# Performance work log

Measured on AMD Instinct MI355X. Metric: run time of the kernel, lower is better.

## Reference

```python
import jax, jax.numpy as jnp
import numpy as np

DIM = 384
HEADS = 12
POS_DIM = (DIM // 4) // 4  # DynamicPosBias: pos_dim = (dim//4)//4 = 24
B_WIN = 64
GH = GW = GD = 8
N_TOK = GH * GW * GD  # 512
NG = 8  # num windows sharing one mask


def _ln(x, g, b):
    m = jnp.mean(x, axis=-1, keepdims=True)
    v = jnp.var(x, axis=-1, keepdims=True)
    return (x - m) / jnp.sqrt(v + 1e-5) * g + b


def setup_inputs() -> dict:
    key = jax.random.key(0)
    ks = jax.random.split(key, 8)
    s = 0.02
    inp = {
        "x": jax.random.normal(ks[0], (B_WIN, N_TOK, DIM), jnp.float32),
        "H": GH, "W": GW, "D": GD,
        "mask": jnp.zeros((NG, N_TOK, N_TOK), jnp.float32),
        "qkv_w": jax.random.normal(ks[1], (DIM, 3 * DIM), jnp.float32) * s,
        "qkv_b": jnp.zeros((3 * DIM,), jnp.float32),
        "proj_w": jax.random.normal(ks[2], (DIM, DIM), jnp.float32) * s,
        "proj_b": jnp.zeros((DIM,), jnp.float32),
        "pos_proj_w": jax.random.normal(ks[3], (3, POS_DIM), jnp.float32) * s,
        "pos_proj_b": jnp.zeros((POS_DIM,), jnp.float32),
        "ln1_g": jnp.ones((POS_DIM,), jnp.float32), "ln1_b": jnp.zeros((POS_DIM,), jnp.float32),
        "pos1_w": jax.random.normal(ks[4], (POS_DIM, POS_DIM), jnp.float32) * s,
        "pos1_b": jnp.zeros((POS_DIM,), jnp.float32),
        "ln2_g": jnp.ones((POS_DIM,), jnp.float32), "ln2_b": jnp.zeros((POS_DIM,), jnp.float32),
        "pos2_w": jax.random.normal(ks[5], (POS_DIM, POS_DIM), jnp.float32) * s,
        "pos2_b": jnp.zeros((POS_DIM,), jnp.float32),
        "ln3_g": jnp.ones((POS_DIM,), jnp.float32), "ln3_b": jnp.zeros((POS_DIM,), jnp.float32),
        "pos3_w": jax.random.normal(ks[6], (POS_DIM, HEADS), jnp.float32) * s,
        "pos3_b": jnp.zeros((HEADS,), jnp.float32),
    }
    return inp


def reference(x, H, W, D, mask, qkv_w, qkv_b, proj_w, proj_b,
              pos_proj_w, pos_proj_b, ln1_g, ln1_b, pos1_w, pos1_b,
              ln2_g, ln2_b, pos2_w, pos2_b, ln3_g, ln3_b, pos3_w, pos3_b):
    B_, N, C = x.shape
    h = HEADS
    d = C // h
    scale = d ** (-0.5)

    qkv = (x @ qkv_w + qkv_b).reshape(B_, N, 3, h, d).transpose(2, 0, 3, 1, 4)
    q, k, v = qkv[0] * scale, qkv[1], qkv[2]  # each (B_, h, N, d)

    attn = jnp.einsum('bhnd,bhmd->bhnm', q, k)  # (B_, h, N, N)

    # dynamic relative position bias
    rh = jnp.arange(1 - H, H)
    rw = jnp.arange(1 - W, W)
    rd = jnp.arange(1 - D, D)
    biases = jnp.stack(jnp.meshgrid(rh, rw, rd, indexing='ij'))
    biases = biases.reshape(3, -1).T.astype(jnp.float32)  # (L, 3), L=(2H-1)(2W-1)(2D-1)

    coords = jnp.stack(jnp.meshgrid(jnp.arange(H), jnp.arange(W), jnp.arange(D), indexing='ij'))
    coords = coords.reshape(3, -1)  # (3, N)
    rel = (coords[:, :, None] - coords[:, None, :]).transpose(1, 2, 0)  # (N, N, 3)
    rel = rel + jnp.array([H - 1, W - 1, D - 1])
    rel = rel * jnp.array([(2 * W - 1) * (2 * D - 1), 2 * D - 1, 1])
    rpi = rel.sum(-1)  # (N, N) int index into L

    pos = biases @ pos_proj_w + pos_proj_b  # (L, pos_dim)
    pos = jax.nn.relu(_ln(pos, ln1_g, ln1_b)) @ pos1_w + pos1_b
    pos = jax.nn.relu(_ln(pos, ln2_g, ln2_b)) @ pos2_w + pos2_b
    pos = jax.nn.relu(_ln(pos, ln3_g, ln3_b)) @ pos3_w + pos3_b  # (L, h)

    rel_bias = pos[rpi]  # (N, N, h)
    attn = attn + rel_bias.transpose(2, 0, 1)[None]  # (B_, h, N, N)

    nG = mask.shape[0]
    attn = attn.reshape(B_ // nG, nG, h, N, N) + mask[None, :, None]
    attn = jax.nn.softmax(attn.reshape(B_, h, N, N), axis=-1)

    out = jnp.einsum('bhnm,bhmd->bhnd', attn, v)  # (B_, h, N, d)
    out = out.transpose(0, 2, 1, 3).reshape(B_, N, C)
    return out @ proj_w + proj_b
```

## Files before the change

### kernel.cpp

```cpp
#include <hip/hip_runtime.h>


typedef __bf16 bf16;
typedef __bf16 bf16x4 __attribute__((ext_vector_type(4)));
typedef __bf16 bf16x8 __attribute__((ext_vector_type(8)));
typedef float  f32x4  __attribute__((ext_vector_type(4)));

#define DIMC   384
#define HEADS  12
#define HD     32
#define NTOK   512
#define NWIN   64
#define LTAB   3375
#define LPAD   3392
#define PD     24
#define SM_SCALE 0.17677669529663687f
#define VSTR   520
#define PSTR   72

#define SZ_WQT  884736ll
#define SZ_WPT  294912ll
#define SZ_POST 81408ll
#define SZ_FLAG 256ll
#define SZ_B2   6291456ll
#define SZ_MT   4194304ll
#define SZ_QKV  25165824ll
#define WS_SMALL 102236160ull
#define WS_BIG   112410368ull

__global__ __launch_bounds__(256) void transpose_kernel(
    const float* __restrict__ src, bf16* __restrict__ dst, int K, int N)
{
    int idx = blockIdx.x * 256 + threadIdx.x;
    if (idx >= K * N) return;
    int n = idx / K, k = idx - n * K;
    dst[idx] = (bf16)src[(size_t)k * N + n];
}

__global__ __launch_bounds__(256) void mask_detect_kernel(
    const float* __restrict__ mask, int* __restrict__ flag)
{
    int i = blockIdx.x * 256 + threadIdx.x;
    const float* p = mask + (size_t)i * 32;
    float s = 0.f;
#pragma unroll
    for (int j = 0; j < 32; j++) s += fabsf(p[j]);
    if (!(s == 0.f)) atomicOr(flag, 1);
}

__device__ inline void ln_relu24(const float* x, const float* __restrict__ g,
                                 const float* __restrict__ b, float* y)
{
    float mean = 0.f;
#pragma unroll
    for (int j = 0; j < PD; j++) mean += x[j];
    mean *= (1.f / PD);
    float var = 0.f;
#pragma unroll
    for (int j = 0; j < PD; j++) { float d = x[j] - mean; var += d * d; }
    var *= (1.f / PD);
    float inv = rsqrtf(var + 1e-5f);
#pragma unroll
    for (int j = 0; j < PD; j++) {
        float t = (x[j] - mean) * inv * g[j] + b[j];
        y[j] = t > 0.f ? t : 0.f;
    }
}

__global__ __launch_bounds__(256) void pos_mlp_kernel(
    const float* __restrict__ pw,  const float* __restrict__ pb,
    const float* __restrict__ g1,  const float* __restrict__ b1,
    const float* __restrict__ w1,  const float* __restrict__ bb1,
    const float* __restrict__ g2,  const float* __restrict__ b2,
    const float* __restrict__ w2,  const float* __restrict__ bb2,
    const float* __restrict__ g3,  const float* __restrict__ b3,
    const float* __restrict__ w3,  const float* __restrict__ bb3,
    bf16* __restrict__ posTg)
{
    int l = blockIdx.x * 256 + threadIdx.x;
    if (l >= LTAB) return;
    int ih = l / 225, iw = (l / 15) % 15, id = l % 15;
    float c0 = (float)(ih - 7), c1 = (float)(iw - 7), c2 = (float)(id - 7);
    float x[PD], y[PD];
#pragma unroll
    for (int j = 0; j < PD; j++)
        x[j] = c0 * pw[j] + c1 * pw[PD + j] + c2 * pw[2 * PD + j] + pb[j];
    ln_relu24(x, g1, b1, y);
#pragma unroll
    for (int j = 0; j < PD; j++) {
        float a = bb1[j];
#pragma unroll
        for (int i = 0; i < PD; i++) a += y[i] * w1[i * PD + j];
        x[j] = a;
    }
    ln_relu24(x, g2, b2, y);
#pragma unroll
    for (int j = 0; j < PD; j++) {
        float a = bb2[j];
#pragma unroll
        for (int i = 0; i < PD; i++) a += y[i] * w2[i * PD + j];
        x[j] = a;
    }
    ln_relu24(x, g3, b3, y);
#pragma unroll
    for (int hh = 0; hh < HEADS; hh++) {
        float a = bb3[hh];
#pragma unroll
        for (int i = 0; i < PD; i++) a += y[i] * w3[i * HEADS + hh];
        posTg[hh * LPAD + l] = (bf16)a;
    }
}

__global__ __launch_bounds__(256) void bias2_build_kernel(
    const bf16* __restrict__ posTg, bf16* __restrict__ bias2)
{
    int idx = blockIdx.x * 256 + threadIdx.x;
    int h = idx >> 18;
    int m = (idx >> 9) & 511;
    int n = idx & 511;
    int dh = (n >> 6) - (m >> 6) + 7;
    int dw = ((n >> 3) & 7) - ((m >> 3) & 7) + 7;
    int dd = (n & 7) - (m & 7) + 7;
    bias2[idx] = posTg[h * LPAD + dh * 225 + dw * 15 + dd];
}

__global__ __launch_bounds__(256) void mt_build_kernel(
    const float* __restrict__ mask, bf16* __restrict__ mt,
    const int* __restrict__ flag)
{
    if (*flag == 0) return;
    __shared__ float tile[64][65];
    const int bx = blockIdx.x;
    const int g  = bx >> 6;
    const int m0 = ((bx >> 3) & 7) * 64;
    const int n0 = (bx & 7) * 64;
    const int tid = threadIdx.x;
#pragma unroll
    for (int k = 0; k < 16; k++) {
        int lin = tid + k * 256;
        int r = lin >> 6, c = lin & 63;
        tile[r][c] = mask[((size_t)g * NTOK + n0 + r) * NTOK + m0 + c];
    }
    __syncthreads();
#pragma unroll
    for (int k = 0; k < 16; k++) {
        int lin = tid + k * 256;
        int mr = lin >> 6, nc = lin & 63;
        mt[((size_t)g * NTOK + m0 + mr) * NTOK + n0 + nc] = (bf16)tile[nc][mr];
    }
}

template <int MODE>
__global__ __launch_bounds__(256) void gemm_bt(
    const void* __restrict__ Av, const bf16* __restrict__ Bt,
    const float* __restrict__ bias,
    bf16* __restrict__ O0, bf16* __restrict__ O1, bf16* __restrict__ O2,
    float* __restrict__ Of, int K, int N)
{
    __shared__ __align__(16) bf16 lA[128 * 64];
    __shared__ __align__(16) bf16 lB[128 * 64];
    const int row0 = blockIdx.x * 128;
    const int col0 = blockIdx.y * 128;
    const int tid  = threadIdx.x;
    const int lane = tid & 63;
    const int wave = tid >> 6;
    const int r0   = (wave >> 1) * 64;
    const int c0   = (wave & 1) * 64;
    const int lrow = lane & 15;
    const int lch  = lane >> 4;

    f32x4 acc[4][4];
    const f32x4 zero4 = {0.f, 0.f, 0.f, 0.f};
#pragma unroll
    for (int i = 0; i < 4; i++)
#pragma unroll
        for (int j = 0; j < 4; j++) acc[i][j] = zero4;

    for (int kt = 0; kt < K; kt += 64) {
        __syncthreads();
#pragma unroll
        for (int it = 0; it < 4; it++) {
            const int c  = tid + it * 256;
            const int rr = c >> 3;
            const int cc = (c & 7) * 8;
            const size_t aoff = (size_t)(row0 + rr) * K + kt + cc;
            if (MODE == 0) {
                const float* Af = (const float*)Av + aoff;
                float4 f0 = *(const float4*)(Af);
                float4 f1 = *(const float4*)(Af + 4);
                bf16x8 v;
                v[0] = (bf16)f0.x; v[1] = (bf16)f0.y; v[2] = (bf16)f0.z; v[3] = (bf16)f0.w;
                v[4] = (bf16)f1.x; v[5] = (bf16)f1.y; v[6] = (bf16)f1.z; v[7] = (bf16)f1.w;
                *(bf16x8*)(lA + c * 8) = v;
            } else {
                *(uint4*)(lA + c * 8) = *(const uint4*)((const bf16*)Av + aoff);
            }
            *(uint4*)(lB + c * 8) = *(const uint4*)(Bt + (size_t)(col0 + rr) * K + kt + cc);
        }
        __syncthreads();
#pragma unroll
        for (int kk = 0; kk < 64; kk += 32) {
            bf16x8 af[4], bfr[4];
#pragma unroll
            for (int i = 0; i < 4; i++)
                af[i] = *(const bf16x8*)(lA + (r0 + i * 16 + lrow) * 64 + kk + lch * 8);
#pragma unroll
            for (int j = 0; j < 4; j++)
                bfr[j] = *(const bf16x8*)(lB + (c0 + j * 16 + lrow) * 64 + kk + lch * 8);
#pragma unroll
            for (int i = 0; i < 4; i++)
#pragma unroll
                for (int j = 0; j < 4; j++)
                    acc[i][j] = __builtin_amdgcn_mfma_f32_16x16x32_bf16(af[i], bfr[j], acc[i][j], 0, 0, 0);
        }
    }

#pragma unroll
    for (int i = 0; i < 4; i++) {
#pragma unroll
        for (int j = 0; j < 4; j++) {
#pragma unroll
            for (int r = 0; r < 4; r++) {
                const int mrow = row0 + r0 + i * 16 + lch * 4 + r;
                const int ncol = col0 + c0 + j * 16 + lrow;
                const float v = acc[i][j][r] + bias[ncol];
                if (MODE == 0) {
                    const int t    = ncol >= 768 ? 2 : (ncol >= 384 ? 1 : 0);
                    const int rem2 = ncol - t * 384;
                    const int hh   = rem2 >> 5;
                    const int dd   = rem2 & 31;
                    const int bwin = mrow >> 9;
                    const int n    = mrow & 511;
                    bf16* dst = (t == 0) ? O0 : ((t == 1) ? O1 : O2);
                    const float vv = (t == 0) ? v * SM_SCALE : v;
                    dst[(size_t)((bwin * HEADS + hh) * NTOK + n) * HD + dd] = (bf16)vv;
                } else {
                    Of[(size_t)mrow * N + ncol] = v;
                }
            }
        }
    }
}

template <int BIG>
__global__ __launch_bounds__(256) void attn_kernel(
    const bf16* __restrict__ Qg, const bf16* __restrict__ Kg,
    const bf16* __restrict__ Vg, const bf16* __restrict__ posTg,
    const float* __restrict__ maskg, const bf16* __restrict__ bias2,
    const bf16* __restrict__ mt, const int* __restrict__ mflag,
    bf16* __restrict__ Og)
{
    __shared__ __align__(16) bf16 lVt[32 * VSTR];
    __shared__ __align__(16) bf16 lP[4 * 32 * PSTR];
    __shared__ __align__(16) bf16 lPos[BIG ? 16 : LPAD];

    const int idx = blockIdx.x;
    const int h   = idx >> 8;
    const int rem = idx & 255;
    const int b   = rem >> 2;
    const int qt  = rem & 3;
    const int g   = b & 7;
    const int tid = threadIdx.x;
    const int lane = tid & 63;
    const int wave = tid >> 6;
    const int lrow = lane & 15;
    const int lch  = lane >> 4;
    const int msk  = *mflag;

    const bf16* Qp = Qg + (size_t)(b * HEADS + h) * NTOK * HD;
    const bf16* Kp = Kg + (size_t)(b * HEADS + h) * NTOK * HD;
    const bf16* Vp = Vg + (size_t)(b * HEADS + h) * NTOK * HD;
    const float* Mp = maskg + (size_t)g * NTOK * NTOK;
    const bf16* B2p = bias2 + (size_t)h * NTOK * NTOK;
    const bf16* Mtp = mt + (size_t)g * NTOK * NTOK;

    for (int n = tid; n < NTOK; n += 256) {
        const bf16* vsrc = Vp + n * HD;
        bf16x8 v0 = *(const bf16x8*)(vsrc);
        bf16x8 v1 = *(const bf16x8*)(vsrc + 8);
        bf16x8 v2 = *(const bf16x8*)(vsrc + 16);
        bf16x8 v3 = *(const bf16x8*)(vsrc + 24);
#pragma unroll
        for (int c = 0; c < 8; c++) {
            lVt[(c)      * VSTR + n] = v0[c];
            lVt[(8 + c)  * VSTR + n] = v1[c];
            lVt[(16 + c) * VSTR + n] = v2[c];
            lVt[(24 + c) * VSTR + n] = v3[c];
        }
    }
    if (!BIG) {
        const uint4* src = (const uint4*)(posTg + h * LPAD);
        for (int i = tid; i < LPAD * 2 / 16; i += 256)
            ((uint4*)lPos)[i] = src[i];
    }
    __syncthreads();

    const int qbase = qt * 128 + wave * 32;

    bf16x8 qf[2];
#pragma unroll
    for (int rt = 0; rt < 2; rt++)
        qf[rt] = *(const bf16x8*)(Qp + (qbase + rt * 16 + lrow) * HD + lch * 8);

    float m_i[2][4], l_i[2][4];
    f32x4 oacc[2][2];
    const f32x4 zero4 = {0.f, 0.f, 0.f, 0.f};
#pragma unroll
    for (int rt = 0; rt < 2; rt++) {
#pragma unroll
        for (int r = 0; r < 4; r++) { m_i[rt][r] = -30.0f; l_i[rt][r] = 0.f; }
        oacc[rt][0] = zero4;
        oacc[rt][1] = zero4;
    }

    bf16* myP = lP + wave * (32 * PSTR);

    for (int kt = 0; kt < 4; kt++) {
        f32x4 sf[2][8];
#pragma unroll
        for (int ct = 0; ct < 8; ct++) {
            bf16x8 kf = *(const bf16x8*)(Kp + (kt * 128 + ct * 16 + lrow) * HD + lch * 8);
#pragma unroll
            for (int rt = 0; rt < 2; rt++)
                sf[rt][ct] = __builtin_amdgcn_mfma_f32_16x16x32_bf16(qf[rt], kf, zero4, 0, 0, 0);
        }

        if (BIG) {
            const int n_base = qbase + lch * 4;
#pragma unroll
            for (int ct = 0; ct < 8; ct++) {
                const int m = kt * 128 + ct * 16 + lrow;
                const size_t tb = (size_t)m * NTOK + n_base;
#pragma unroll
                for (int rt = 0; rt < 2; rt++) {
                    bf16x4 bv = *(const bf16x4*)(B2p + tb + rt * 16);
#pragma unroll
                    for (int r = 0; r < 4; r++)
                        sf[rt][ct][r] += (float)bv[r];
                }
                if (msk) {
#pragma unroll
                    for (int rt = 0; rt < 2; rt++) {
                        bf16x4 mv = *(const bf16x4*)(Mtp + tb + rt * 16);
#pragma unroll
                        for (int r = 0; r < 4; r++)
                            sf[rt][ct][r] += (float)mv[r];
                    }
                }
            }
        } else {
            const int mb = kt * 128 + lrow;
#pragma unroll
            for (int rt = 0; rt < 2; rt++) {
#pragma unroll
                for (int r = 0; r < 4; r++) {
                    const int row = qbase + rt * 16 + lch * 4 + r;
                    const int nh = row >> 6, nw = (row >> 3) & 7, nd = row & 7;
                    const float* mp = Mp + (size_t)row * NTOK + mb;
#pragma unroll
                    for (int ct = 0; ct < 8; ct++) {
                        const int m  = mb + ct * 16;
                        const int rpi = (nh - (m >> 6) + 7) * 225
                                      + (nw - ((m >> 3) & 7) + 7) * 15
                                      + (nd - (m & 7) + 7);
                        sf[rt][ct][r] += (float)lPos[rpi];
                        if (msk) sf[rt][ct][r] += mp[ct * 16];
                    }
                }
            }
        }

#pragma unroll
        for (int rt = 0; rt < 2; rt++) {
#pragma unroll
            for (int r = 0; r < 4; r++) {
                float mx = sf[rt][0][r];
#pragma unroll
                for (int ct = 1; ct < 8; ct++) mx = fmaxf(mx, sf[rt][ct][r]);
                mx = fmaxf(mx, __shfl_xor(mx, 1));
                mx = fmaxf(mx, __shfl_xor(mx, 2));
                mx = fmaxf(mx, __shfl_xor(mx, 4));
                mx = fmaxf(mx, __shfl_xor(mx, 8));
                const float mold  = m_i[rt][r];
                const float mnew  = fmaxf(mold, mx);
                const float alpha = __expf(mold - mnew);
                m_i[rt][r] = mnew;
                float ls = 0.f;
#pragma unroll
                for (int ct = 0; ct < 8; ct++) {
                    float p = __expf(sf[rt][ct][r] - mnew);
                    ls += p;
                    sf[rt][ct][r] = p;
                }
                ls += __shfl_xor(ls, 1);
                ls += __shfl_xor(ls, 2);
                ls += __shfl_xor(ls, 4);
                ls += __shfl_xor(ls, 8);
                l_i[rt][r] = l_i[rt][r] * alpha + ls;
                oacc[rt][0][r] *= alpha;
                oacc[rt][1][r] *= alpha;
            }
        }

#pragma unroll
        for (int hf = 0; hf < 2; hf++) {
#pragma unroll
            for (int rt = 0; rt < 2; rt++)
#pragma unroll
                for (int r = 0; r < 4; r++) {
                    const int prow = (rt * 16 + lch * 4 + r) * PSTR + lrow;
#pragma unroll
                    for (int c4 = 0; c4 < 4; c4++)
                        myP[prow + c4 * 16] = (bf16)sf[rt][hf * 4 + c4][r];
                }
#pragma unroll
            for (int k2 = 0; k2 < 2; k2++) {
                const int mofs = kt * 128 + hf * 64 + k2 * 32;
                bf16x8 bv[2];
#pragma unroll
                for (int ct = 0; ct < 2; ct++)
                    bv[ct] = *(const bf16x8*)(lVt + (ct * 16 + lrow) * VSTR + mofs + lch * 8);
#pragma unroll
                for (int rt = 0; rt < 2; rt++) {
                    bf16x8 ap = *(const bf16x8*)(myP + (rt * 16 + lrow) * PSTR + k2 * 32 + lch * 8);
#pragma unroll
                    for (int ct = 0; ct < 2; ct++)
                        oacc[rt][ct] = __builtin_amdgcn_mfma_f32_16x16x32_bf16(ap, bv[ct], oacc[rt][ct], 0, 0, 0);
                }
            }
        }
    }

#pragma unroll
    for (int rt = 0; rt < 2; rt++) {
#pragma unroll
        for (int r = 0; r < 4; r++) {
            const int n = qbase + rt * 16 + lch * 4 + r;
            const float inv = 1.f / fmaxf(l_i[rt][r], 1e-20f);
            bf16* orow = Og + (size_t)(b * NTOK + n) * DIMC + h * HD;
#pragma unroll
            for (int ct = 0; ct < 2; ct++)
                orow[ct * 16 + lrow] = (bf16)(oacc[rt][ct][r] * inv);
        }
    }
}

extern "C" void kernel_launch(void* const* d_in, const int* in_sizes, int n_in,
                              void* d_out, int out_size, void* d_ws, size_t ws_size,
                              hipStream_t stream)
{
    if (ws_size < WS_SMALL) return;
    const bool BIG = (ws_size >= WS_BIG);

    const float* x      = (const float*)d_in[0];
    const float* maskp  = (const float*)d_in[4];
    const float* qkv_w  = (const float*)d_in[5];
    const float* qkv_b  = (const float*)d_in[6];
    const float* proj_w = (const float*)d_in[7];
    const float* proj_b = (const float*)d_in[8];

    char* ws = (char*)d_ws;
    size_t off = 0;
    bf16* wsWqT  = (bf16*)(ws + off); off += SZ_WQT;
    bf16* wsWpT  = (bf16*)(ws + off); off += SZ_WPT;
    bf16* wsPosT = (bf16*)(ws + off); off += SZ_POST;
    int*  wsFlag = (int*)(ws + off);  off += SZ_FLAG;
    bf16* wsB2 = nullptr; bf16* wsMt = nullptr;
    if (BIG) {
        wsB2 = (bf16*)(ws + off); off += SZ_B2;
        wsMt = (bf16*)(ws + off); off += SZ_MT;
    } else {
        off = 1572864;
    }
    bf16* wsQ    = (bf16*)(ws + off); off += SZ_QKV;
    bf16* wsK    = (bf16*)(ws + off); off += SZ_QKV;
    bf16* wsV    = (bf16*)(ws + off); off += SZ_QKV;
    bf16* wsAttn = (bf16*)(ws + off);

    hipMemsetAsync(wsFlag, 0, 4, stream);
    mask_detect_kernel<<<256, 256, 0, stream>>>(maskp, wsFlag);

    transpose_kernel<<<(384 * 1152 + 255) / 256, 256, 0, stream>>>(qkv_w, wsWqT, 384, 1152);
    transpose_kernel<<<(384 * 384 + 255) / 256, 256, 0, stream>>>(proj_w, wsWpT, 384, 384);
    pos_mlp_kernel<<<(LTAB + 255) / 256, 256, 0, stream>>>(
        (const float*)d_in[9],  (const float*)d_in[10], (const float*)d_in[11],
        (const float*)d_in[12], (const float*)d_in[13], (const float*)d_in[14],
        (const float*)d_in[15], (const float*)d_in[16], (const float*)d_in[17],
        (const float*)d_in[18], (const float*)d_in[19], (const float*)d_in[20],
        (const float*)d_in[21], (const float*)d_in[22], wsPosT);

    if (BIG) {
        bias2_build_kernel<<<(HEADS * NTOK * NTOK) / 256, 256, 0, stream>>>(wsPosT, wsB2);
        mt_build_kernel<<<8 * 64, 256, 0, stream>>>(maskp, wsMt, wsFlag);
    }

    gemm_bt<0><<<dim3(256, 9), 256, 0, stream>>>(x, wsWqT, qkv_b, wsQ, wsK, wsV,
                                                 nullptr, 384, 1152);

    if (BIG)
        attn_kernel<1><<<HEADS * NWIN * 4, 256, 0, stream>>>(
            wsQ, wsK, wsV, wsPosT, maskp, wsB2, wsMt, wsFlag, wsAttn);
    else
        attn_kernel<0><<<HEADS * NWIN * 4, 256, 0, stream>>>(
            wsQ, wsK, wsV, wsPosT, maskp, wsB2, wsMt, wsFlag, wsAttn);

    gemm_bt<1><<<dim3(256, 3), 256, 0, stream>>>(wsAttn, wsWpT, proj_b,
                                                 nullptr, nullptr, nullptr,
                                                 (float*)d_out, 384, 384);
}
```

Measured before the change: 452.6 us.

## Keep attention probabilities in registers via transposed S and permlane packing

Several changes land together. The attention kernel now computes S transposed (K times Q), so each lane holds one query column, and it reduces the row max and sum across 16-lane groups. It packs the probabilities into bf16 MFMA operands with cvt_pk and permlane swaps instead of writing them to a shared-memory P buffer. Softmax switches to exp2, with log2e folded into the Q scale, the position bias and the mask. Separately, x is cast to bf16 by its own kernel so the GEMMs can use direct global-to-LDS loads, and the transposed-mask build kernel is removed because the mask is now read in its natural row layout. Together this adds an extra pass over x and some register pressure, set against a 4-blocks-per-CU launch bound.

```diff
diff --git a/kernel.cpp b/kernel.cpp
--- a/kernel.cpp
+++ b/kernel.cpp
@@ -5,6 +5,8 @@
 typedef __bf16 bf16x4 __attribute__((ext_vector_type(4)));
 typedef __bf16 bf16x8 __attribute__((ext_vector_type(8)));
 typedef float  f32x4  __attribute__((ext_vector_type(4)));
+typedef unsigned int u32;
+typedef u32 u32x4v __attribute__((ext_vector_type(4)));
 
 #define DIMC   384
 #define HEADS  12
@@ -14,9 +16,9 @@
 #define LTAB   3375
 #define LPAD   3392
 #define PD     24
-#define SM_SCALE 0.17677669529663687f
+#define LOG2E  1.4426950408889634f
+#define QPRE   (0.17677669529663687f * LOG2E)
 #define VSTR   520
-#define PSTR   72
 
 #define SZ_WQT  884736ll
 #define SZ_WPT  294912ll
@@ -28,6 +30,30 @@
 #define WS_SMALL 102236160ull
 #define WS_BIG   112410368ull
 
+__device__ inline u32 cvtpk(float lo, float hi) {
+    u32 r;
+    asm("v_cvt_pk_bf16_f32 %0, %1, %2" : "=v"(r) : "v"(lo), "v"(hi));
+    return r;
+}
+__device__ inline void plswap32(u32& a, u32& b) {
+    asm("v_permlane32_swap_b32 %0, %1" : "+v"(a), "+v"(b));
+}
+__device__ inline void plswap16(u32& a, u32& b) {
+    asm("v_permlane16_swap_b32 %0, %1" : "+v"(a), "+v"(b));
+}
+__device__ inline float ex2(float x) {
+#if __has_builtin(__builtin_amdgcn_exp2f)
+    return __builtin_amdgcn_exp2f(x);
+#else
+    float r; asm("v_exp_f32 %0, %1" : "=v"(r) : "v"(x)); return r;
+#endif
+}
+__device__ inline void gload_lds16(const void* g, void* l) {
+    __builtin_amdgcn_global_load_lds(
+        (const __attribute__((address_space(1))) void*)g,
+        (__attribute__((address_space(3))) void*)l, 16, 0, 0);
+}
+
 __global__ __launch_bounds__(256) void transpose_kernel(
     const float* __restrict__ src, bf16* __restrict__ dst, int K, int N)
 {
@@ -35,6 +61,17 @@
     if (idx >= K * N) return;
     int n = idx / K, k = idx - n * K;
     dst[idx] = (bf16)src[(size_t)k * N + n];
+}
+
+__global__ __launch_bounds__(256) void xcast_kernel(
+    const float* __restrict__ src, bf16* __restrict__ dst)
+{
+    const int i = blockIdx.x * 256 + threadIdx.x;
+    const f32x4 v = *(const f32x4*)(src + (size_t)i * 4);
+    bf16x4 o;
+#pragma unroll
+    for (int j = 0; j < 4; j++) o[j] = (bf16)v[j];
+    *(bf16x4*)(dst + (size_t)i * 4) = o;
 }
 
 __global__ __launch_bounds__(256) void mask_detect_kernel(
@@ -107,7 +144,7 @@
         float a = bb3[hh];
 #pragma unroll
         for (int i = 0; i < PD; i++) a += y[i] * w3[i * HEADS + hh];
-        posTg[hh * LPAD + l] = (bf16)a;
+        posTg[hh * LPAD + l] = (bf16)(a * LOG2E);
     }
 }
 
@@ -116,43 +153,17 @@
 {
     int idx = blockIdx.x * 256 + threadIdx.x;
     int h = idx >> 18;
-    int m = (idx >> 9) & 511;
-    int n = idx & 511;
-    int dh = (n >> 6) - (m >> 6) + 7;
-    int dw = ((n >> 3) & 7) - ((m >> 3) & 7) + 7;
-    int dd = (n & 7) - (m & 7) + 7;
+    int q = (idx >> 9) & 511;
+    int m = idx & 511;
+    int dh = (q >> 6) - (m >> 6) + 7;
+    int dw = ((q >> 3) & 7) - ((m >> 3) & 7) + 7;
+    int dd = (q & 7) - (m & 7) + 7;
     bias2[idx] = posTg[h * LPAD + dh * 225 + dw * 15 + dd];
-}
-
-__global__ __launch_bounds__(256) void mt_build_kernel(
-    const float* __restrict__ mask, bf16* __restrict__ mt,
-    const int* __restrict__ flag)
-{
-    if (*flag == 0) return;
-    __shared__ float tile[64][65];
-    const int bx = blockIdx.x;
-    const int g  = bx >> 6;
-    const int m0 = ((bx >> 3) & 7) * 64;
-    const int n0 = (bx & 7) * 64;
-    const int tid = threadIdx.x;
-#pragma unroll
-    for (int k = 0; k < 16; k++) {
-        int lin = tid + k * 256;
-        int r = lin >> 6, c = lin & 63;
-        tile[r][c] = mask[((size_t)g * NTOK + n0 + r) * NTOK + m0 + c];
-    }
-    __syncthreads();
-#pragma unroll
-    for (int k = 0; k < 16; k++) {
-        int lin = tid + k * 256;
-        int mr = lin >> 6, nc = lin & 63;
-        mt[((size_t)g * NTOK + m0 + mr) * NTOK + n0 + nc] = (bf16)tile[nc][mr];
-    }
 }
 
 template <int MODE>
 __global__ __launch_bounds__(256) void gemm_bt(
-    const void* __restrict__ Av, const bf16* __restrict__ Bt,
+    const bf16* __restrict__ A, const bf16* __restrict__ Bt,
     const float* __restrict__ bias,
     bf16* __restrict__ O0, bf16* __restrict__ O1, bf16* __restrict__ O2,
     float* __restrict__ Of, int K, int N)
@@ -183,19 +194,10 @@
             const int c  = tid + it * 256;
             const int rr = c >> 3;
             const int cc = (c & 7) * 8;
-            const size_t aoff = (size_t)(row0 + rr) * K + kt + cc;
-            if (MODE == 0) {
-                const float* Af = (const float*)Av + aoff;
-                float4 f0 = *(const float4*)(Af);
-                float4 f1 = *(const float4*)(Af + 4);
-                bf16x8 v;
-                v[0] = (bf16)f0.x; v[1] = (bf16)f0.y; v[2] = (bf16)f0.z; v[3] = (bf16)f0.w;
-                v[4] = (bf16)f1.x; v[5] = (bf16)f1.y; v[6] = (bf16)f1.z; v[7] = (bf16)f1.w;
-                *(bf16x8*)(lA + c * 8) = v;
-            } else {
-                *(uint4*)(lA + c * 8) = *(const uint4*)((const bf16*)Av + aoff);
-            }
-            *(uint4*)(lB + c * 8) = *(const uint4*)(Bt + (size_t)(col0 + rr) * K + kt + cc);
+            bf16* la = lA + (size_t)(it * 256 + wave * 64) * 8;
+            bf16* lb = lB + (size_t)(it * 256 + wave * 64) * 8;
+            gload_lds16(A  + (size_t)(row0 + rr) * K + kt + cc, la);
+            gload_lds16(Bt + (size_t)(col0 + rr) * K + kt + cc, lb);
         }
         __syncthreads();
 #pragma unroll
@@ -232,7 +234,7 @@
                     const int bwin = mrow >> 9;
                     const int n    = mrow & 511;
                     bf16* dst = (t == 0) ? O0 : ((t == 1) ? O1 : O2);
-                    const float vv = (t == 0) ? v * SM_SCALE : v;
+                    const float vv = (t == 0) ? v * QPRE : v;
                     dst[(size_t)((bwin * HEADS + hh) * NTOK + n) * HD + dd] = (bf16)vv;
                 } else {
                     Of[(size_t)mrow * N + ncol] = v;
@@ -243,15 +245,13 @@
 }
 
 template <int BIG>
-__global__ __launch_bounds__(256) void attn_kernel(
+__global__ __launch_bounds__(256, 4) void attn_kernel(
     const bf16* __restrict__ Qg, const bf16* __restrict__ Kg,
     const bf16* __restrict__ Vg, const bf16* __restrict__ posTg,
     const float* __restrict__ maskg, const bf16* __restrict__ bias2,
-    const bf16* __restrict__ mt, const int* __restrict__ mflag,
-    bf16* __restrict__ Og)
+    const int* __restrict__ mflag, bf16* __restrict__ Og)
 {
     __shared__ __align__(16) bf16 lVt[32 * VSTR];
-    __shared__ __align__(16) bf16 lP[4 * 32 * PSTR];
     __shared__ __align__(16) bf16 lPos[BIG ? 16 : LPAD];
 
     const int idx = blockIdx.x;
@@ -267,12 +267,11 @@
     const int lch  = lane >> 4;
     const int msk  = *mflag;
 
-    const bf16* Qp = Qg + (size_t)(b * HEADS + h) * NTOK * HD;
-    const bf16* Kp = Kg + (size_t)(b * HEADS + h) * NTOK * HD;
-    const bf16* Vp = Vg + (size_t)(b * HEADS + h) * NTOK * HD;
+    const bf16* Qp  = Qg + (size_t)(b * HEADS + h) * NTOK * HD;
+    const bf16* Kp  = Kg + (size_t)(b * HEADS + h) * NTOK * HD;
+    const bf16* Vp  = Vg + (size_t)(b * HEADS + h) * NTOK * HD;
     const float* Mp = maskg + (size_t)g * NTOK * NTOK;
     const bf16* B2p = bias2 + (size_t)h * NTOK * NTOK;
-    const bf16* Mtp = mt + (size_t)g * NTOK * NTOK;
 
     for (int n = tid; n < NTOK; n += 256) {
         const bf16* vsrc = Vp + n * HD;
@@ -299,148 +298,151 @@
 
     bf16x8 qf[2];
 #pragma unroll
-    for (int rt = 0; rt < 2; rt++)
-        qf[rt] = *(const bf16x8*)(Qp + (qbase + rt * 16 + lrow) * HD + lch * 8);
-
-    float m_i[2][4], l_i[2][4];
+    for (int t = 0; t < 2; t++)
+        qf[t] = *(const bf16x8*)(Qp + (size_t)(qbase + t * 16 + lrow) * HD + lch * 8);
+
+    int qc0[2] = {0, 0}, qc1[2] = {0, 0}, qc2[2] = {0, 0};
+    if (!BIG) {
+#pragma unroll
+        for (int t = 0; t < 2; t++) {
+            const int q = qbase + t * 16 + lrow;
+            qc0[t] = q >> 6; qc1[t] = (q >> 3) & 7; qc2[t] = q & 7;
+        }
+    }
+
+    float m_i[2] = {-1e30f, -1e30f};
+    float l_i[2] = {0.f, 0.f};
     f32x4 oacc[2][2];
     const f32x4 zero4 = {0.f, 0.f, 0.f, 0.f};
-#pragma unroll
-    for (int rt = 0; rt < 2; rt++) {
-#pragma unroll
-        for (int r = 0; r < 4; r++) { m_i[rt][r] = -30.0f; l_i[rt][r] = 0.f; }
-        oacc[rt][0] = zero4;
-        oacc[rt][1] = zero4;
-    }
-
-    bf16* myP = lP + wave * (32 * PSTR);
+    oacc[0][0] = zero4; oacc[0][1] = zero4;
+    oacc[1][0] = zero4; oacc[1][1] = zero4;
 
     for (int kt = 0; kt < 4; kt++) {
-        f32x4 sf[2][8];
-#pragma unroll
-        for (int ct = 0; ct < 8; ct++) {
-            bf16x8 kf = *(const bf16x8*)(Kp + (kt * 128 + ct * 16 + lrow) * HD + lch * 8);
-#pragma unroll
-            for (int rt = 0; rt < 2; rt++)
-                sf[rt][ct] = __builtin_amdgcn_mfma_f32_16x16x32_bf16(qf[rt], kf, zero4, 0, 0, 0);
-        }
-
-        if (BIG) {
-            const int n_base = qbase + lch * 4;
+        bf16x8 apc[2][4];
+        float alr[2];
+
+#pragma unroll
+        for (int t = 0; t < 2; t++) {
+            const int qrow = qbase + t * 16 + lrow;
+            f32x4 sf[8];
+
+            bf16x4 bld[8];
+            if (BIG) {
+                const bf16* brow = B2p + (size_t)qrow * NTOK + kt * 128 + lch * 4;
+#pragma unroll
+                for (int ct = 0; ct < 8; ct++)
+                    bld[ct] = *(const bf16x4*)(brow + ct * 16);
+            }
+
 #pragma unroll
             for (int ct = 0; ct < 8; ct++) {
-                const int m = kt * 128 + ct * 16 + lrow;
-                const size_t tb = (size_t)m * NTOK + n_base;
-#pragma unroll
-                for (int rt = 0; rt < 2; rt++) {
-                    bf16x4 bv = *(const bf16x4*)(B2p + tb + rt * 16);
+                bf16x8 kf = *(const bf16x8*)(Kp + (size_t)(kt * 128 + ct * 16 + lrow) * HD + lch * 8);
+                sf[ct] = __builtin_amdgcn_mfma_f32_16x16x32_bf16(kf, qf[t], zero4, 0, 0, 0);
+            }
+
+            if (BIG) {
+#pragma unroll
+                for (int ct = 0; ct < 8; ct++)
 #pragma unroll
                     for (int r = 0; r < 4; r++)
-                        sf[rt][ct][r] += (float)bv[r];
-                }
-                if (msk) {
-#pragma unroll
-                    for (int rt = 0; rt < 2; rt++) {
-                        bf16x4 mv = *(const bf16x4*)(Mtp + tb + rt * 16);
-#pragma unroll
-                        for (int r = 0; r < 4; r++)
-                            sf[rt][ct][r] += (float)mv[r];
+                        sf[ct][r] += (float)bld[ct][r];
+            } else {
+#pragma unroll
+                for (int ct = 0; ct < 8; ct++) {
+#pragma unroll
+                    for (int r = 0; r < 4; r++) {
+                        const int k = kt * 128 + ct * 16 + lch * 4 + r;
+                        const int rpi = (qc0[t] - (k >> 6) + 7) * 225
+                                      + (qc1[t] - ((k >> 3) & 7) + 7) * 15
+                                      + (qc2[t] - (k & 7) + 7);
+                        sf[ct][r] += (float)lPos[rpi];
                     }
                 }
             }
-        } else {
-            const int mb = kt * 128 + lrow;
-#pragma unroll
-            for (int rt = 0; rt < 2; rt++) {
-#pragma unroll
-                for (int r = 0; r < 4; r++) {
-                    const int row = qbase + rt * 16 + lch * 4 + r;
-                    const int nh = row >> 6, nw = (row >> 3) & 7, nd = row & 7;
-                    const float* mp = Mp + (size_t)row * NTOK + mb;
-#pragma unroll
-                    for (int ct = 0; ct < 8; ct++) {
-                        const int m  = mb + ct * 16;
-                        const int rpi = (nh - (m >> 6) + 7) * 225
-                                      + (nw - ((m >> 3) & 7) + 7) * 15
-                                      + (nd - (m & 7) + 7);
-                        sf[rt][ct][r] += (float)lPos[rpi];
-                        if (msk) sf[rt][ct][r] += mp[ct * 16];
-                    }
+            if (msk) {
+                const float* mrow = Mp + (size_t)qrow * NTOK + kt * 128 + lch * 4;
+#pragma unroll
+                for (int ct = 0; ct < 8; ct++) {
+                    f32x4 mv = *(const f32x4*)(mrow + ct * 16);
+#pragma unroll
+                    for (int r = 0; r < 4; r++)
+                        sf[ct][r] = fmaf(mv[r], LOG2E, sf[ct][r]);
                 }
             }
-        }
-
-#pragma unroll
-        for (int rt = 0; rt < 2; rt++) {
+
+            float px[8];
+#pragma unroll
+            for (int ct = 0; ct < 8; ct++)
+                px[ct] = fmaxf(fmaxf(sf[ct][0], sf[ct][1]), fmaxf(sf[ct][2], sf[ct][3]));
+            float mx = fmaxf(fmaxf(fmaxf(px[0], px[1]), fmaxf(px[2], px[3])),
+                             fmaxf(fmaxf(px[4], px[5]), fmaxf(px[6], px[7])));
+            mx = fmaxf(mx, __shfl_xor(mx, 16));
+            mx = fmaxf(mx, __shfl_xor(mx, 32));
+            const float mnew = fmaxf(m_i[t], mx);
+            const float al   = ex2(m_i[t] - mnew);
+            m_i[t] = mnew;
+            alr[t] = al;
+
+            float s0 = 0.f, s1 = 0.f;
+#pragma unroll
+            for (int ct = 0; ct < 8; ct++) {
+#pragma unroll
+                for (int r = 0; r < 4; r++)
+                    sf[ct][r] = ex2(sf[ct][r] - mnew);
+                s0 += sf[ct][0] + sf[ct][1];
+                s1 += sf[ct][2] + sf[ct][3];
+            }
+            float ls = s0 + s1;
+            ls += __shfl_xor(ls, 16);
+            ls += __shfl_xor(ls, 32);
+            l_i[t] = l_i[t] * al + ls;
+
+#pragma unroll
+            for (int c2 = 0; c2 < 4; c2++) {
+                u32 a01 = cvtpk(sf[2 * c2][0],     sf[2 * c2][1]);
+                u32 a23 = cvtpk(sf[2 * c2][2],     sf[2 * c2][3]);
+                u32 b01 = cvtpk(sf[2 * c2 + 1][0], sf[2 * c2 + 1][1]);
+                u32 b23 = cvtpk(sf[2 * c2 + 1][2], sf[2 * c2 + 1][3]);
+                plswap32(a01, b01); plswap16(a01, b01);
+                plswap32(a23, b23); plswap16(a23, b23);
+                u32x4v w; w[0] = a01; w[1] = a23; w[2] = b01; w[3] = b23;
+                apc[t][c2] = __builtin_bit_cast(bf16x8, w);
+            }
+        }
+
+#pragma unroll
+        for (int t = 0; t < 2; t++) {
 #pragma unroll
             for (int r = 0; r < 4; r++) {
-                float mx = sf[rt][0][r];
-#pragma unroll
-                for (int ct = 1; ct < 8; ct++) mx = fmaxf(mx, sf[rt][ct][r]);
-                mx = fmaxf(mx, __shfl_xor(mx, 1));
-                mx = fmaxf(mx, __shfl_xor(mx, 2));
-                mx = fmaxf(mx, __shfl_xor(mx, 4));
-                mx = fmaxf(mx, __shfl_xor(mx, 8));
-                const float mold  = m_i[rt][r];
-                const float mnew  = fmaxf(mold, mx);
-                const float alpha = __expf(mold - mnew);
-                m_i[rt][r] = mnew;
-                float ls = 0.f;
-#pragma unroll
-                for (int ct = 0; ct < 8; ct++) {
-                    float p = __expf(sf[rt][ct][r] - mnew);
-                    ls += p;
-                    sf[rt][ct][r] = p;
-                }
-                ls += __shfl_xor(ls, 1);
-                ls += __shfl_xor(ls, 2);
-                ls += __shfl_xor(ls, 4);
-                ls += __shfl_xor(ls, 8);
-                l_i[rt][r] = l_i[rt][r] * alpha + ls;
-                oacc[rt][0][r] *= alpha;
-                oacc[rt][1][r] *= alpha;
-            }
-        }
-
-#pragma unroll
-        for (int hf = 0; hf < 2; hf++) {
-#pragma unroll
-            for (int rt = 0; rt < 2; rt++)
-#pragma unroll
-                for (int r = 0; r < 4; r++) {
-                    const int prow = (rt * 16 + lch * 4 + r) * PSTR + lrow;
-#pragma unroll
-                    for (int c4 = 0; c4 < 4; c4++)
-                        myP[prow + c4 * 16] = (bf16)sf[rt][hf * 4 + c4][r];
-                }
-#pragma unroll
-            for (int k2 = 0; k2 < 2; k2++) {
-                const int mofs = kt * 128 + hf * 64 + k2 * 32;
-                bf16x8 bv[2];
-#pragma unroll
-                for (int ct = 0; ct < 2; ct++)
-                    bv[ct] = *(const bf16x8*)(lVt + (ct * 16 + lrow) * VSTR + mofs + lch * 8);
-#pragma unroll
-                for (int rt = 0; rt < 2; rt++) {
-                    bf16x8 ap = *(const bf16x8*)(myP + (rt * 16 + lrow) * PSTR + k2 * 32 + lch * 8);
-#pragma unroll
-                    for (int ct = 0; ct < 2; ct++)
-                        oacc[rt][ct] = __builtin_amdgcn_mfma_f32_16x16x32_bf16(ap, bv[ct], oacc[rt][ct], 0, 0, 0);
-                }
-            }
-        }
-    }
-
-#pragma unroll
-    for (int rt = 0; rt < 2; rt++) {
+                const float a = __shfl(alr[t], lch * 4 + r);
+                oacc[t][0][r] *= a;
+                oacc[t][1][r] *= a;
+            }
+        }
+
+#pragma unroll
+        for (int c2 = 0; c2 < 4; c2++) {
+            const int mofs = kt * 128 + c2 * 32;
+            bf16x8 bv0 = *(const bf16x8*)(lVt + (size_t)lrow * VSTR + mofs + lch * 8);
+            bf16x8 bv1 = *(const bf16x8*)(lVt + (size_t)(16 + lrow) * VSTR + mofs + lch * 8);
+#pragma unroll
+            for (int t = 0; t < 2; t++) {
+                oacc[t][0] = __builtin_amdgcn_mfma_f32_16x16x32_bf16(apc[t][c2], bv0, oacc[t][0], 0, 0, 0);
+                oacc[t][1] = __builtin_amdgcn_mfma_f32_16x16x32_bf16(apc[t][c2], bv1, oacc[t][1], 0, 0, 0);
+            }
+        }
+    }
+
+#pragma unroll
+    for (int t = 0; t < 2; t++) {
 #pragma unroll
         for (int r = 0; r < 4; r++) {
-            const int n = qbase + rt * 16 + lch * 4 + r;
-            const float inv = 1.f / fmaxf(l_i[rt][r], 1e-20f);
+            const float lv  = __shfl(l_i[t], lch * 4 + r);
+            const float inv = 1.f / fmaxf(lv, 1e-20f);
+            const int n = qbase + t * 16 + lch * 4 + r;
             bf16* orow = Og + (size_t)(b * NTOK + n) * DIMC + h * HD;
-#pragma unroll
-            for (int ct = 0; ct < 2; ct++)
-                orow[ct * 16 + lrow] = (bf16)(oacc[rt][ct][r] * inv);
+            orow[lrow]      = (bf16)(oacc[t][0][r] * inv);
+            orow[16 + lrow] = (bf16)(oacc[t][1][r] * inv);
         }
     }
 }
@@ -465,10 +467,10 @@
     bf16* wsWpT  = (bf16*)(ws + off); off += SZ_WPT;
     bf16* wsPosT = (bf16*)(ws + off); off += SZ_POST;
     int*  wsFlag = (int*)(ws + off);  off += SZ_FLAG;
-    bf16* wsB2 = nullptr; bf16* wsMt = nullptr;
+    bf16* wsB2 = nullptr;
     if (BIG) {
         wsB2 = (bf16*)(ws + off); off += SZ_B2;
-        wsMt = (bf16*)(ws + off); off += SZ_MT;
+        off += SZ_MT;
     } else {
         off = 1572864;
     }
@@ -476,6 +478,7 @@
     bf16* wsK    = (bf16*)(ws + off); off += SZ_QKV;
     bf16* wsV    = (bf16*)(ws + off); off += SZ_QKV;
     bf16* wsAttn = (bf16*)(ws + off);
+    bf16* wsXb   = wsAttn;
 
     hipMemsetAsync(wsFlag, 0, 4, stream);
     mask_detect_kernel<<<256, 256, 0, stream>>>(maskp, wsFlag);
@@ -489,20 +492,20 @@
         (const float*)d_in[18], (const float*)d_in[19], (const float*)d_in[20],
         (const float*)d_in[21], (const float*)d_in[22], wsPosT);
 
-    if (BIG) {
+    xcast_kernel<<<(32768 * 384 / 4) / 256, 256, 0, stream>>>(x, wsXb);
+
+    if (BIG)
         bias2_build_kernel<<<(HEADS * NTOK * NTOK) / 256, 256, 0, stream>>>(wsPosT, wsB2);
-        mt_build_kernel<<<8 * 64, 256, 0, stream>>>(maskp, wsMt, wsFlag);
-    }
-
-    gemm_bt<0><<<dim3(256, 9), 256, 0, stream>>>(x, wsWqT, qkv_b, wsQ, wsK, wsV,
+
+    gemm_bt<0><<<dim3(256, 9), 256, 0, stream>>>(wsXb, wsWqT, qkv_b, wsQ, wsK, wsV,
                                                  nullptr, 384, 1152);
 
     if (BIG)
         attn_kernel<1><<<HEADS * NWIN * 4, 256, 0, stream>>>(
-            wsQ, wsK, wsV, wsPosT, maskp, wsB2, wsMt, wsFlag, wsAttn);
+            wsQ, wsK, wsV, wsPosT, maskp, wsB2, wsFlag, wsAttn);
     else
         attn_kernel<0><<<HEADS * NWIN * 4, 256, 0, stream>>>(
-            wsQ, wsK, wsV, wsPosT, maskp, wsB2, wsMt, wsFlag, wsAttn);
+            wsQ, wsK, wsV, wsPosT, maskp, wsB2, wsFlag, wsAttn);
 
     gemm_bt<1><<<dim3(256, 3), 256, 0, stream>>>(wsAttn, wsWpT, proj_b,
                                                  nullptr, nullptr, nullptr,
```

New measurement: 422.0 us. 1.07x faster.
